# Performance work log

Measured on AMD Instinct MI355X. Metric: run time of the kernel, lower is better.

Reference implementation:

```python
import jax, jax.numpy as jnp
import numpy as np
from jax import lax

CR = 16        # opt.cr (temporal dim)
HEADS = 4      # num_heads
DIM = 64       # dim == channel count c
B = 2          # true batch; input batch = B*CR
H = W = 128


def setup_inputs() -> dict:
    key = jax.random.key(0)
    k1, k2, k3, k4 = jax.random.split(key, 4)
    return {
        "x": jax.random.normal(k1, (B * CR, DIM, H, W), jnp.float32),
        "ln_weight": jnp.ones((DIM,), jnp.float32),
        "ln_bias": jnp.zeros((DIM,), jnp.float32),
        "qkv_w": jax.random.normal(k2, (3 * CR, CR), jnp.float32) * 0.05,   # 1x1 conv
        "dw_w": jax.random.normal(k3, (3 * CR, 1, 3, 3), jnp.float32) * 0.1,  # depthwise 3x3
        "proj_w": jax.random.normal(k4, (DIM, DIM), jnp.float32) * 0.05,   # 1x1 conv
        "temperature": jnp.ones((HEADS, 1, 1), jnp.float32),
    }


def reference(x, ln_weight, ln_bias, qkv_w, dw_w, proj_w, temperature):
    b, c, h, w = x.shape
    Bt = b // CR
    # WithBias LayerNorm over channel dim (per spatial location), eps=1e-5
    mu = jnp.mean(x, axis=1, keepdims=True)
    var = jnp.mean(jnp.square(x - mu), axis=1, keepdims=True)
    xn = (x - mu) / jnp.sqrt(var + 1e-5)
    xn = xn * ln_weight[None, :, None, None] + ln_bias[None, :, None, None]
    # (B*cr, c, h, w) -> (B, cr, c, h, w) -> (B*c, cr, h, w)
    x_in = xn.reshape(Bt, CR, c, h, w).transpose(0, 2, 1, 3, 4).reshape(Bt * c, CR, h, w)
    # 1x1 qkv conv (no bias)
    qkv = jnp.einsum('oc,bchw->bohw', qkv_w, x_in)
    # depthwise 3x3 conv, padding 1
    qkv = lax.conv_general_dilated(qkv, dw_w, (1, 1), 'SAME',
                                   feature_group_count=3 * CR,
                                   dimension_numbers=('NCHW', 'OIHW', 'NCHW'))
    q, k, v = jnp.split(qkv, 3, axis=1)
    ch = CR // HEADS  # per-head channel dim

    def heads(t):
        return t.reshape(Bt * c, HEADS, ch, h * w)

    def l2n(t):
        n = jnp.sqrt(jnp.sum(jnp.square(t), axis=-1, keepdims=True))
        return t / jnp.maximum(n, 1e-12)

    q, k, v = heads(q), heads(k), heads(v)
    q, k = l2n(q), l2n(k)
    # transposed (channel) attention: small ch x ch scores
    attn = jnp.einsum('bhcn,bhdn->bhcd', q, k) * temperature[None]
    attn = jax.nn.softmax(attn, axis=-1)
    out = jnp.einsum('bhcd,bhdn->bhcn', attn, v)  # (B*c, heads, ch, hw)
    # (B*c, cr, h, w) -> (B, c, cr, h, w) -> (B*cr, c, h, w)
    out = out.reshape(Bt * c, CR, h, w).reshape(Bt, c, CR, h, w)
    out = out.transpose(0, 2, 1, 3, 4).reshape(b, c, h, w)
    # 1x1 project_out
    return jnp.einsum('oc,bchw->bohw', proj_w, out)
```

## Files before the change

### kernel.cpp

```cpp
#include <hip/hip_runtime.h>
#include <hip/hip_fp16.h>

typedef _Float16 half8_t __attribute__((ext_vector_type(8)));
typedef float float4_t __attribute__((ext_vector_type(4)));

__device__ __forceinline__ float2 h2f2(unsigned int u) {
  return __half22float2(__builtin_bit_cast(__half2, u));
}
__device__ __forceinline__ unsigned int f2h2(float a, float b) {
  return __builtin_bit_cast(unsigned int, __floats2half2_rn(a, b));
}

#if __has_builtin(__builtin_amdgcn_fdot2)
typedef _Float16 h2v __attribute__((ext_vector_type(2)));
__device__ __forceinline__ float fdot2(unsigned int a, unsigned int b, float c) {
  return __builtin_amdgcn_fdot2(__builtin_bit_cast(h2v, a),
                                __builtin_bit_cast(h2v, b), c, false);
}
#else
__device__ __forceinline__ float fdot2(unsigned int a, unsigned int b, float c) {
  float2 fa = h2f2(a), fb = h2f2(b);
  return fmaf(fa.y, fb.y, fmaf(fa.x, fb.x, c));
}
#endif

__global__ __launch_bounds__(256) void k_stats(
    const float2* __restrict__ x2, float4* __restrict__ stats4,
    const float* __restrict__ qkvw, const float* __restrict__ dww,
    const float* __restrict__ projw, unsigned int* __restrict__ qkvpk,
    unsigned int* __restrict__ dwpk, unsigned int* __restrict__ projpk) {
  if (blockIdx.x >= 1024) {
    for (int t = threadIdx.x; t < 2648; t += 256) {
      if (t < 2048) {
        int o = t >> 5, c2 = t & 31;
        projpk[t] = f2h2(projw[(o << 6) + 2 * c2], projw[(o << 6) + 2 * c2 + 1]);
      } else if (t < 2432) {
        int i = t - 2048;
        int ch = i >> 3, tp = i & 7;
        qkvpk[i] = f2h2(qkvw[(ch << 4) + 2 * tp], qkvw[(ch << 4) + 2 * tp + 1]);
      } else {
        int i = t - 2432;
        int pl = i / 9, k = i - pl * 9;
        dwpk[i] = f2h2(dww[18 * pl + k], dww[18 * pl + 9 + k]);
      }
    }
    return;
  }
  int id = blockIdx.x * 256 + threadIdx.x;
  int bb = id >> 13;
  int jp = id & 8191;
  const float2* xp = x2 + ((size_t)bb << 19) + jp;
  float s0 = 0.f, q0 = 0.f, s1 = 0.f, q1 = 0.f;
#pragma unroll
  for (int ci = 0; ci < 64; ++ci) {
    float2 v = xp[(size_t)ci << 13];
    s0 += v.x; q0 = fmaf(v.x, v.x, q0);
    s1 += v.y; q1 = fmaf(v.y, v.y, q1);
  }
  float mu0 = s0 * (1.f / 64.f), mu1 = s1 * (1.f / 64.f);
  float4 r;
  r.x = mu0; r.y = rsqrtf(fmaf(-mu0, mu0, q0 * (1.f / 64.f)) + 1e-5f);
  r.z = mu1; r.w = rsqrtf(fmaf(-mu1, mu1, q1 * (1.f / 64.f)) + 1e-5f);
  stats4[id] = r;
}

__global__ __launch_bounds__(256) void k_xn(
    const float2* __restrict__ x2, const float4* __restrict__ stats4,
    const float* __restrict__ lnw, const float* __restrict__ lnb,
    unsigned int* __restrict__ xnw) {
  int bc = blockIdx.y, bt = bc >> 6, ci = bc & 63;
  int jp = blockIdx.x * 256 + threadIdx.x;
  float lw = lnw[ci], lb = lnb[ci];
  unsigned int w0[8], w1[8];
#pragma unroll
  for (int tp = 0; tp < 8; ++tp) {
    int bb0 = (bt << 4) + 2 * tp;
    float2 xa = x2[(((size_t)((bb0 << 6) + ci)) << 13) + jp];
    float2 xb = x2[(((size_t)(((bb0 + 1) << 6) + ci)) << 13) + jp];
    float4 sa = stats4[((size_t)bb0 << 13) + jp];
    float4 sb = stats4[((size_t)(bb0 + 1) << 13) + jp];
    w0[tp] = f2h2(fmaf((xa.x - sa.x) * sa.y, lw, lb),
                  fmaf((xb.x - sb.x) * sb.y, lw, lb));
    w1[tp] = f2h2(fmaf((xa.y - sa.z) * sa.w, lw, lb),
                  fmaf((xb.y - sb.z) * sb.w, lw, lb));
  }
  size_t base = (((size_t)bc << 14) + 2 * (size_t)jp) * 8;
  *reinterpret_cast<uint4*>(&xnw[base + 0]) = make_uint4(w0[0], w0[1], w0[2], w0[3]);
  *reinterpret_cast<uint4*>(&xnw[base + 4]) = make_uint4(w0[4], w0[5], w0[6], w0[7]);
  *reinterpret_cast<uint4*>(&xnw[base + 8]) = make_uint4(w1[0], w1[1], w1[2], w1[3]);
  *reinterpret_cast<uint4*>(&xnw[base + 12]) = make_uint4(w1[4], w1[5], w1[6], w1[7]);
}

__global__ __launch_bounds__(256) void k_fused(
    const unsigned int* __restrict__ xnw, const unsigned int* __restrict__ qkvpk,
    const unsigned int* __restrict__ dwpk, unsigned int* __restrict__ vbuf,
    float* __restrict__ Sacc, float* __restrict__ Nacc) {
  __shared__ unsigned int pre[3232];
  __shared__ unsigned int qk[2080];
  int tid = threadIdx.x;
  int bc = blockIdx.y;
  int tx0 = (blockIdx.x & 3) << 5;
  int ty0 = (blockIdx.x >> 2) << 3;
  int lane15 = tid & 15;
  int kg = (tid >> 4) & 3;
  int wv = tid >> 6;
  int jx = tid & 7, iy = (tid >> 3) & 7;

  uint4 bfr[6];
  int pwa[6];
#pragma unroll
  for (int i = 0; i < 6; ++i) {
    int T = wv + 4 * i;
    int hp = T * 16 + lane15;
    int hy = hp / 36, hx = hp - hy * 36;
    int gy = ty0 + hy - 1, gx = tx0 + hx - 2;
    bool val = hp < 360;
    bool ok = val && ((unsigned)gy < 128u) && ((unsigned)gx < 128u);
    pwa[i] = val ? (hy * 40 + hx) : -1;
    uint4 bw = make_uint4(0, 0, 0, 0);
    if (ok && kg < 2)
      bw = *reinterpret_cast<const uint4*>(
          &xnw[((size_t)bc << 17) + (size_t)((gy << 7) + gx) * 8 + 4 * kg]);
    bfr[i] = bw;
  }

  for (int m = 0; m < 3; ++m) {
    if (m > 0) {
      int pm = m - 1;
      {
        int combo = tid >> 3, pc = tid & 7;
        int hp_ = combo >> 4, cd = combo & 15, cc = cd >> 2, dd = cd & 3;
        const unsigned int* qrow = qk + (4 * hp_ + cc) * 130;
        const unsigned int* krow = qk + (8 + 4 * hp_ + dd) * 130;
        float s = 0.f;
#pragma unroll
        for (int i = 0; i < 8; ++i) {
          uint2 q2 = *reinterpret_cast<const uint2*>(&qrow[2 * pc + (i << 4)]);
          uint2 k2 = *reinterpret_cast<const uint2*>(&krow[2 * pc + (i << 4)]);
          s = fdot2(q2.x, k2.x, s);
          s = fdot2(q2.y, k2.y, s);
        }
        s += __shfl_xor(s, 1); s += __shfl_xor(s, 2); s += __shfl_xor(s, 4);
        if (pc == 0)
          atomicAdd(&Sacc[((bc << 2) + 2 * pm + hp_) * 16 + cc * 4 + dd], s);
      }
      {
        int row = tid >> 4, pc = tid & 15;
        const unsigned int* rp = qk + row * 130;
        float n = 0.f;
#pragma unroll
        for (int i = 0; i < 4; ++i) {
          uint2 v2 = *reinterpret_cast<const uint2*>(&rp[2 * pc + (i << 5)]);
          n = fdot2(v2.x, v2.x, n);
          n = fdot2(v2.y, v2.y, n);
        }
        n += __shfl_xor(n, 1); n += __shfl_xor(n, 2);
        n += __shfl_xor(n, 4); n += __shfl_xor(n, 8);
        if (pc == 0) {
          int g = (row < 8) ? (8 * pm + row) : (16 + 8 * pm + (row - 8));
          atomicAdd(&Nacc[(bc << 5) + g], n);
        }
      }
    }
    {
      int gch = (m < 2)
                    ? ((lane15 < 8) ? (8 * m + lane15) : (16 + 8 * m + (lane15 - 8)))
                    : (32 + lane15);
      uint4 aw = make_uint4(0, 0, 0, 0);
      if (kg < 2) aw = *reinterpret_cast<const uint4*>(&qkvpk[gch * 8 + 4 * kg]);
      half8_t af = __builtin_bit_cast(half8_t, aw);
      float4_t zz = {0.f, 0.f, 0.f, 0.f};
#pragma unroll
      for (int i = 0; i < 6; ++i) {
        half8_t bf = __builtin_bit_cast(half8_t, bfr[i]);
        float4_t d = __builtin_amdgcn_mfma_f32_16x16x32_f16(af, bf, zz, 0, 0, 0);
        if (pwa[i] >= 0) {
          pre[(2 * kg) * 404 + pwa[i]] = f2h2(d[0], d[1]);
          pre[(2 * kg + 1) * 404 + pwa[i]] = f2h2(d[2], d[3]);
        }
      }
    }
    __syncthreads();
    unsigned int vs[2][4];
#pragma unroll
    for (int p2 = 0; p2 < 2; ++p2) {
      int pl = 2 * wv + p2;
      int gpl = (m < 2) ? ((pl < 4) ? (4 * m + pl) : (8 + 4 * m + (pl - 4)))
                        : (16 + pl);
      const unsigned int* wp = dwpk + gpl * 9;
      __half2 a0 = __floats2half2_rn(0.f, 0.f), a1 = a0, a2 = a0, a3 = a0;
      int base = pl * 404 + iy * 40 + 4 * jx;
#pragma unroll
      for (int dy = 0; dy < 3; ++dy) {
        uint4 C0 = *reinterpret_cast<const uint4*>(&pre[base + dy * 40]);
        uint4 C1 = *reinterpret_cast<const uint4*>(&pre[base + dy * 40 + 4]);
        __half2 c1 = __builtin_bit_cast(__half2, C0.y);
        __half2 c2 = __builtin_bit_cast(__half2, C0.z);
        __half2 c3 = __builtin_bit_cast(__half2, C0.w);
        __half2 c4 = __builtin_bit_cast(__half2, C1.x);
        __half2 c5 = __builtin_bit_cast(__half2, C1.y);
        __half2 c6 = __builtin_bit_cast(__half2, C1.z);
        __half2 w0 = __builtin_bit_cast(__half2, wp[dy * 3 + 0]);
        __half2 w1 = __builtin_bit_cast(__half2, wp[dy * 3 + 1]);
        __half2 w2 = __builtin_bit_cast(__half2, wp[dy * 3 + 2]);
        a0 = __hfma2(w0, c1, a0); a0 = __hfma2(w1, c2, a0); a0 = __hfma2(w2, c3, a0);
        a1 = __hfma2(w0, c2, a1); a1 = __hfma2(w1, c3, a1); a1 = __hfma2(w2, c4, a1);
        a2 = __hfma2(w0, c3, a2); a2 = __hfma2(w1, c4, a2); a2 = __hfma2(w2, c5, a2);
        a3 = __hfma2(w0, c4, a3); a3 = __hfma2(w1, c5, a3); a3 = __hfma2(w2, c6, a3);
      }
      unsigned int u0 = __builtin_bit_cast(unsigned int, a0);
      unsigned int u1 = __builtin_bit_cast(unsigned int, a1);
      unsigned int u2 = __builtin_bit_cast(unsigned int, a2);
      unsigned int u3 = __builtin_bit_cast(unsigned int, a3);
      if (m < 2) {
        uint2 E, O;
        E.x = (u0 & 0xFFFFu) | (u1 << 16);
        E.y = (u2 & 0xFFFFu) | (u3 << 16);
        O.x = (u0 >> 16) | (u1 & 0xFFFF0000u);
        O.y = (u2 >> 16) | (u3 & 0xFFFF0000u);
        int pp = iy * 16 + 2 * jx;
        *reinterpret_cast<uint2*>(&qk[(2 * pl) * 130 + pp]) = E;
        *reinterpret_cast<uint2*>(&qk[(2 * pl + 1) * 130 + pp]) = O;
      } else {
        vs[p2][0] = u0; vs[p2][1] = u1; vs[p2][2] = u2; vs[p2][3] = u3;
      }
    }
    if (m == 2) {
      size_t vb2 = (((size_t)(bc * 4 + wv)) << 15) +
                   (size_t)(((ty0 + iy) << 7) + tx0 + 4 * jx) * 2;
      *reinterpret_cast<uint4*>(&vbuf[vb2]) =
          make_uint4(vs[0][0], vs[1][0], vs[0][1], vs[1][1]);
      *reinterpret_cast<uint4*>(&vbuf[vb2 + 4]) =
          make_uint4(vs[0][2], vs[1][2], vs[0][3], vs[1][3]);
    } else {
      __syncthreads();
    }
  }
}

__global__ __launch_bounds__(256) void k_outproj(
    const unsigned int* __restrict__ vbuf, const float* __restrict__ Sacc,
    const float* __restrict__ Nacc, const float* __restrict__ temp,
    const unsigned int* __restrict__ projpk, float* __restrict__ out) {
  __shared__ unsigned int Yl[32 * 260];
  __shared__ unsigned int attn_l[128];
  int tid = threadIdx.x;
  int comb = blockIdx.y;
  int bt = comb >> 4, hd = (comb >> 2) & 3, c = comb & 3;
  int lane15 = tid & 15;
  int kg = (tid >> 4) & 3;
  int wv = tid >> 6;

  if (tid < 64) {
    int b = (bt << 6) + tid;
    float tp = temp[hd];
    float iq = 1.f / fmaxf(sqrtf(Nacc[(b << 5) + (hd << 2) + c]), 1e-12f);
    float l[4];
#pragma unroll
    for (int d = 0; d < 4; ++d) {
      float ik = 1.f / fmaxf(sqrtf(Nacc[(b << 5) + 16 + (hd << 2) + d]), 1e-12f);
      l[d] = Sacc[((b << 2) + hd) * 16 + c * 4 + d] * iq * ik * tp;
    }
    float mx = fmaxf(fmaxf(l[0], l[1]), fmaxf(l[2], l[3]));
    float e0 = expf(l[0] - mx), e1 = expf(l[1] - mx);
    float e2 = expf(l[2] - mx), e3 = expf(l[3] - mx);
    float inv = 1.f / (e0 + e1 + e2 + e3);
    attn_l[2 * tid] = f2h2(e0 * inv, e1 * inv);
    attn_l[2 * tid + 1] = f2h2(e2 * inv, e3 * inv);
  }
  __syncthreads();

  {
    int gpx = (blockIdx.x << 8) + tid;
    size_t vb = (((size_t)(bt * 256 + hd)) << 15) + (size_t)gpx * 2;
#pragma unroll
    for (int ci2 = 0; ci2 < 32; ++ci2) {
      uint2 A0 = *reinterpret_cast<const uint2*>(&vbuf[vb + ((size_t)(2 * ci2) << 17)]);
      uint2 A1 = *reinterpret_cast<const uint2*>(&vbuf[vb + ((size_t)(2 * ci2 + 1) << 17)]);
      uint4 aw = *reinterpret_cast<const uint4*>(&attn_l[4 * ci2]);
      float y0 = fdot2(A0.x, aw.x, fdot2(A0.y, aw.y, 0.f));
      float y1 = fdot2(A1.x, aw.z, fdot2(A1.y, aw.w, 0.f));
      Yl[ci2 * 260 + tid] = f2h2(y0, y1);
    }
  }
  __syncthreads();

  half8_t A0[4], A1[4];
#pragma unroll
  for (int ot = 0; ot < 4; ++ot) {
    A0[ot] = __builtin_bit_cast(
        half8_t, *reinterpret_cast<const uint4*>(
                     &projpk[(ot * 16 + lane15) * 32 + kg * 4]));
    A1[ot] = __builtin_bit_cast(
        half8_t, *reinterpret_cast<const uint4*>(
                     &projpk[(ot * 16 + lane15) * 32 + 16 + kg * 4]));
  }
  float4_t zz = {0.f, 0.f, 0.f, 0.f};
  size_t outbase = ((size_t)comb << 20) + (blockIdx.x << 8);
#pragma unroll
  for (int pt = 0; pt < 4; ++pt) {
    int pxl = wv * 64 + pt * 16 + lane15;
    unsigned int r0 = Yl[(kg * 4 + 0) * 260 + pxl];
    unsigned int r1 = Yl[(kg * 4 + 1) * 260 + pxl];
    unsigned int r2 = Yl[(kg * 4 + 2) * 260 + pxl];
    unsigned int r3 = Yl[(kg * 4 + 3) * 260 + pxl];
    half8_t B0 = __builtin_bit_cast(half8_t, make_uint4(r0, r1, r2, r3));
    unsigned int s0 = Yl[(16 + kg * 4 + 0) * 260 + pxl];
    unsigned int s1 = Yl[(16 + kg * 4 + 1) * 260 + pxl];
    unsigned int s2 = Yl[(16 + kg * 4 + 2) * 260 + pxl];
    unsigned int s3 = Yl[(16 + kg * 4 + 3) * 260 + pxl];
    half8_t B1 = __builtin_bit_cast(half8_t, make_uint4(s0, s1, s2, s3));
#pragma unroll
    for (int ot = 0; ot < 4; ++ot) {
      float4_t d = __builtin_amdgcn_mfma_f32_16x16x32_f16(A0[ot], B0, zz, 0, 0, 0);
      d = __builtin_amdgcn_mfma_f32_16x16x32_f16(A1[ot], B1, d, 0, 0, 0);
      int o0 = ot * 16 + kg * 4;
#pragma unroll
      for (int r = 0; r < 4; ++r)
        out[outbase + ((size_t)(o0 + r) << 14) + pxl] = d[r];
    }
  }
}

extern "C" void kernel_launch(void* const* d_in, const int* in_sizes, int n_in,
                              void* d_out, int out_size, void* d_ws, size_t ws_size,
                              hipStream_t stream) {
  const float* x = (const float*)d_in[0];
  const float* lnw = (const float*)d_in[1];
  const float* lnb = (const float*)d_in[2];
  const float* qkvw = (const float*)d_in[3];
  const float* dww = (const float*)d_in[4];
  const float* projw = (const float*)d_in[5];
  const float* temp = (const float*)d_in[6];
  float* out = (float*)d_out;

  unsigned int* xnw = (unsigned int*)d_ws;
  unsigned int* vbuf = xnw + (67108864ull / 4);
  char* tail = (char*)d_ws + 134217728ull;
  float4* stats4 = (float4*)tail;
  float* Sacc = (float*)(tail + 4194304ull);
  float* Nacc = Sacc + 8192;
  unsigned int* projpk = (unsigned int*)(Nacc + 4096);
  unsigned int* qkvpk = projpk + 2048;
  unsigned int* dwpk = qkvpk + 384;

  hipMemsetAsync(Sacc, 0, (8192 + 4096) * sizeof(float), stream);
  k_stats<<<dim3(1025), dim3(256), 0, stream>>>((const float2*)x, stats4, qkvw,
                                                dww, projw, qkvpk, dwpk, projpk);
  k_xn<<<dim3(32, 128), dim3(256), 0, stream>>>((const float2*)x, stats4, lnw,
                                                lnb, xnw);
  k_fused<<<dim3(64, 128), dim3(256), 0, stream>>>(xnw, qkvpk, dwpk, vbuf, Sacc,
                                                   Nacc);
  k_outproj<<<dim3(64, 32), dim3(256), 0, stream>>>(vbuf, Sacc, Nacc, temp,
                                                    projpk, out);
}
```

Measured before the change: 223.4 us.

## Enlarge fused qkv/dwconv tile to 32x16 and remap depthwise conv per-thread

```diff
diff --git a/kernel.cpp b/kernel.cpp
--- a/kernel.cpp
+++ b/kernel.cpp
@@ -95,28 +95,25 @@
     const unsigned int* __restrict__ xnw, const unsigned int* __restrict__ qkvpk,
     const unsigned int* __restrict__ dwpk, unsigned int* __restrict__ vbuf,
     float* __restrict__ Sacc, float* __restrict__ Nacc) {
-  __shared__ unsigned int pre[3232];
-  __shared__ unsigned int qk[2080];
+  __shared__ unsigned int pre[8 * 612];
+  __shared__ unsigned int qk[16 * 258];
   int tid = threadIdx.x;
   int bc = blockIdx.y;
   int tx0 = (blockIdx.x & 3) << 5;
-  int ty0 = (blockIdx.x >> 2) << 3;
+  int ty0 = (blockIdx.x >> 2) << 4;
   int lane15 = tid & 15;
   int kg = (tid >> 4) & 3;
   int wv = tid >> 6;
-  int jx = tid & 7, iy = (tid >> 3) & 7;
-
-  uint4 bfr[6];
-  int pwa[6];
-#pragma unroll
-  for (int i = 0; i < 6; ++i) {
-    int T = wv + 4 * i;
-    int hp = T * 16 + lane15;
-    int hy = hp / 36, hx = hp - hy * 36;
-    int gy = ty0 + hy - 1, gx = tx0 + hx - 2;
-    bool val = hp < 360;
-    bool ok = val && ((unsigned)gy < 128u) && ((unsigned)gx < 128u);
-    pwa[i] = val ? (hy * 40 + hx) : -1;
+  int iy = tid >> 4, jx = tid & 15;
+  int dwbase = iy * 34 + 2 * jx;
+
+  uint4 bfr[10];
+#pragma unroll
+  for (int i = 0; i < 10; ++i) {
+    int hp = (wv + 4 * i) * 16 + lane15;
+    int hy = hp / 34, hx = hp - hy * 34;
+    int gy = ty0 + hy - 1, gx = tx0 + hx - 1;
+    bool ok = (hp < 612) && ((unsigned)gy < 128u) && ((unsigned)gx < 128u);
     uint4 bw = make_uint4(0, 0, 0, 0);
     if (ok && kg < 2)
       bw = *reinterpret_cast<const uint4*>(
@@ -130,11 +127,11 @@
       {
         int combo = tid >> 3, pc = tid & 7;
         int hp_ = combo >> 4, cd = combo & 15, cc = cd >> 2, dd = cd & 3;
-        const unsigned int* qrow = qk + (4 * hp_ + cc) * 130;
-        const unsigned int* krow = qk + (8 + 4 * hp_ + dd) * 130;
+        const unsigned int* qrow = qk + (4 * hp_ + cc) * 258;
+        const unsigned int* krow = qk + (8 + 4 * hp_ + dd) * 258;
         float s = 0.f;
 #pragma unroll
-        for (int i = 0; i < 8; ++i) {
+        for (int i = 0; i < 16; ++i) {
           uint2 q2 = *reinterpret_cast<const uint2*>(&qrow[2 * pc + (i << 4)]);
           uint2 k2 = *reinterpret_cast<const uint2*>(&krow[2 * pc + (i << 4)]);
           s = fdot2(q2.x, k2.x, s);
@@ -146,10 +143,10 @@
       }
       {
         int row = tid >> 4, pc = tid & 15;
-        const unsigned int* rp = qk + row * 130;
+        const unsigned int* rp = qk + row * 258;
         float n = 0.f;
 #pragma unroll
-        for (int i = 0; i < 4; ++i) {
+        for (int i = 0; i < 8; ++i) {
           uint2 v2 = *reinterpret_cast<const uint2*>(&rp[2 * pc + (i << 5)]);
           n = fdot2(v2.x, v2.x, n);
           n = fdot2(v2.y, v2.y, n);
@@ -171,69 +168,59 @@
       half8_t af = __builtin_bit_cast(half8_t, aw);
       float4_t zz = {0.f, 0.f, 0.f, 0.f};
 #pragma unroll
-      for (int i = 0; i < 6; ++i) {
+      for (int i = 0; i < 10; ++i) {
+        int hp = (wv + 4 * i) * 16 + lane15;
         half8_t bf = __builtin_bit_cast(half8_t, bfr[i]);
         float4_t d = __builtin_amdgcn_mfma_f32_16x16x32_f16(af, bf, zz, 0, 0, 0);
-        if (pwa[i] >= 0) {
-          pre[(2 * kg) * 404 + pwa[i]] = f2h2(d[0], d[1]);
-          pre[(2 * kg + 1) * 404 + pwa[i]] = f2h2(d[2], d[3]);
+        if (hp < 612) {
+          pre[(2 * kg) * 612 + hp] = f2h2(d[0], d[1]);
+          pre[(2 * kg + 1) * 612 + hp] = f2h2(d[2], d[3]);
         }
       }
     }
     __syncthreads();
-    unsigned int vs[2][4];
-#pragma unroll
-    for (int p2 = 0; p2 < 2; ++p2) {
-      int pl = 2 * wv + p2;
+    unsigned int vs0[8], vs1[8];
+#pragma unroll
+    for (int pl = 0; pl < 8; ++pl) {
       int gpl = (m < 2) ? ((pl < 4) ? (4 * m + pl) : (8 + 4 * m + (pl - 4)))
                         : (16 + pl);
       const unsigned int* wp = dwpk + gpl * 9;
-      __half2 a0 = __floats2half2_rn(0.f, 0.f), a1 = a0, a2 = a0, a3 = a0;
-      int base = pl * 404 + iy * 40 + 4 * jx;
+      __half2 a0 = __floats2half2_rn(0.f, 0.f), a1 = a0;
+      int base = pl * 612 + dwbase;
 #pragma unroll
       for (int dy = 0; dy < 3; ++dy) {
-        uint4 C0 = *reinterpret_cast<const uint4*>(&pre[base + dy * 40]);
-        uint4 C1 = *reinterpret_cast<const uint4*>(&pre[base + dy * 40 + 4]);
-        __half2 c1 = __builtin_bit_cast(__half2, C0.y);
-        __half2 c2 = __builtin_bit_cast(__half2, C0.z);
-        __half2 c3 = __builtin_bit_cast(__half2, C0.w);
-        __half2 c4 = __builtin_bit_cast(__half2, C1.x);
-        __half2 c5 = __builtin_bit_cast(__half2, C1.y);
-        __half2 c6 = __builtin_bit_cast(__half2, C1.z);
+        uint2 A = *reinterpret_cast<const uint2*>(&pre[base + dy * 34]);
+        uint2 B = *reinterpret_cast<const uint2*>(&pre[base + dy * 34 + 2]);
+        __half2 d0 = __builtin_bit_cast(__half2, A.x);
+        __half2 d1 = __builtin_bit_cast(__half2, A.y);
+        __half2 d2 = __builtin_bit_cast(__half2, B.x);
+        __half2 d3 = __builtin_bit_cast(__half2, B.y);
         __half2 w0 = __builtin_bit_cast(__half2, wp[dy * 3 + 0]);
         __half2 w1 = __builtin_bit_cast(__half2, wp[dy * 3 + 1]);
         __half2 w2 = __builtin_bit_cast(__half2, wp[dy * 3 + 2]);
-        a0 = __hfma2(w0, c1, a0); a0 = __hfma2(w1, c2, a0); a0 = __hfma2(w2, c3, a0);
-        a1 = __hfma2(w0, c2, a1); a1 = __hfma2(w1, c3, a1); a1 = __hfma2(w2, c4, a1);
-        a2 = __hfma2(w0, c3, a2); a2 = __hfma2(w1, c4, a2); a2 = __hfma2(w2, c5, a2);
-        a3 = __hfma2(w0, c4, a3); a3 = __hfma2(w1, c5, a3); a3 = __hfma2(w2, c6, a3);
+        a0 = __hfma2(w0, d0, a0); a0 = __hfma2(w1, d1, a0); a0 = __hfma2(w2, d2, a0);
+        a1 = __hfma2(w0, d1, a1); a1 = __hfma2(w1, d2, a1); a1 = __hfma2(w2, d3, a1);
       }
       unsigned int u0 = __builtin_bit_cast(unsigned int, a0);
       unsigned int u1 = __builtin_bit_cast(unsigned int, a1);
-      unsigned int u2 = __builtin_bit_cast(unsigned int, a2);
-      unsigned int u3 = __builtin_bit_cast(unsigned int, a3);
       if (m < 2) {
-        uint2 E, O;
-        E.x = (u0 & 0xFFFFu) | (u1 << 16);
-        E.y = (u2 & 0xFFFFu) | (u3 << 16);
-        O.x = (u0 >> 16) | (u1 & 0xFFFF0000u);
-        O.y = (u2 >> 16) | (u3 & 0xFFFF0000u);
-        int pp = iy * 16 + 2 * jx;
-        *reinterpret_cast<uint2*>(&qk[(2 * pl) * 130 + pp]) = E;
-        *reinterpret_cast<uint2*>(&qk[(2 * pl + 1) * 130 + pp]) = O;
+        qk[(2 * pl) * 258 + tid]     = (u0 & 0xFFFFu) | (u1 << 16);
+        qk[(2 * pl + 1) * 258 + tid] = (u0 >> 16) | (u1 & 0xFFFF0000u);
       } else {
-        vs[p2][0] = u0; vs[p2][1] = u1; vs[p2][2] = u2; vs[p2][3] = u3;
-      }
-    }
-    if (m == 2) {
-      size_t vb2 = (((size_t)(bc * 4 + wv)) << 15) +
-                   (size_t)(((ty0 + iy) << 7) + tx0 + 4 * jx) * 2;
-      *reinterpret_cast<uint4*>(&vbuf[vb2]) =
-          make_uint4(vs[0][0], vs[1][0], vs[0][1], vs[1][1]);
-      *reinterpret_cast<uint4*>(&vbuf[vb2 + 4]) =
-          make_uint4(vs[0][2], vs[1][2], vs[0][3], vs[1][3]);
+        vs0[pl] = u0;
+        vs1[pl] = u1;
+      }
+    }
+    if (m < 2) {
+      __syncthreads();
     } else {
-      __syncthreads();
+      int px0 = ((ty0 + iy) << 7) + tx0 + 2 * jx;
+#pragma unroll
+      for (int hg = 0; hg < 4; ++hg) {
+        size_t a = (((size_t)(bc * 4 + hg)) << 15) + (size_t)px0 * 2;
+        *reinterpret_cast<uint4*>(&vbuf[a]) =
+            make_uint4(vs0[2 * hg], vs0[2 * hg + 1], vs1[2 * hg], vs1[2 * hg + 1]);
+      }
     }
   }
 }
@@ -349,7 +336,7 @@
                                                 dww, projw, qkvpk, dwpk, projpk);
   k_xn<<<dim3(32, 128), dim3(256), 0, stream>>>((const float2*)x, stats4, lnw,
                                                 lnb, xnw);
-  k_fused<<<dim3(64, 128), dim3(256), 0, stream>>>(xnw, qkvpk, dwpk, vbuf, Sacc,
+  k_fused<<<dim3(32, 128), dim3(256), 0, stream>>>(xnw, qkvpk, dwpk, vbuf, Sacc,
                                                    Nacc);
   k_outproj<<<dim3(64, 32), dim3(256), 0, stream>>>(vbuf, Sacc, Nacc, temp,
                                                     projpk, out);
```

After: 192.5 us. 1.16x faster.
